# Performance work log

Measured on AMD Instinct MI355X. Metric: run time of the kernel, lower is better.

The kernel has to match this reference:

```python
import itertools
import jax, jax.numpy as jnp
import numpy as np

H, W, DIM, NH, WS = 64, 64, 384, 12, 7
HD = DIM // NH            # head dim = key_dim (attn_ratio=1)
N = WS * WS               # tokens per window
SCALE = HD ** -0.5
EPS = 1e-5
BATCH = 4
HID = int(DIM * 4.0)


def _bias_idxs():
    points = list(itertools.product(range(WS), range(WS)))
    offsets, idxs = {}, []
    for p1 in points:
        for p2 in points:
            off = (abs(p1[0] - p2[0]), abs(p1[1] - p2[1]))
            if off not in offsets:
                offsets[off] = len(offsets)
            idxs.append(offsets[off])
    return np.asarray(idxs, dtype=np.int32).reshape(N, N)

BIAS_IDXS = _bias_idxs()              # [N, N] static
NUM_OFFSETS = int(BIAS_IDXS.max()) + 1  # 49 for a 7x7 window


def setup_inputs() -> dict:
    key = jax.random.key(0)
    ks = jax.random.split(key, 10)
    rn = lambda k, shp, s=0.02: jax.random.normal(k, shp, jnp.float32) * s
    return {
        "x": jax.random.normal(ks[0], (BATCH, H * W, DIM), jnp.float32),
        "ln1_g": jnp.ones((DIM,), jnp.float32),
        "ln1_b": jnp.zeros((DIM,), jnp.float32),
        "qkv_w": rn(ks[1], (DIM, 3 * DIM)),
        "qkv_b": jnp.zeros((3 * DIM,), jnp.float32),
        "proj_w": rn(ks[2], (DIM, DIM)),
        "proj_b": jnp.zeros((DIM,), jnp.float32),
        "attn_bias": rn(ks[3], (NH, NUM_OFFSETS), 0.1),
        "conv_w": rn(ks[4], (DIM, 1, 3, 3), 0.1),  # depthwise OIHW
        "bn_g": jnp.ones((DIM,), jnp.float32),
        "bn_b": jnp.zeros((DIM,), jnp.float32),
        "bn_mean": rn(ks[5], (DIM,), 0.05),
        "bn_var": jax.random.uniform(ks[6], (DIM,), jnp.float32, 0.5, 1.5),
        "ln2_g": jnp.ones((DIM,), jnp.float32),
        "ln2_b": jnp.zeros((DIM,), jnp.float32),
        "fc1_w": rn(ks[7], (DIM, HID)),
        "fc1_b": jnp.zeros((HID,), jnp.float32),
        "fc2_w": rn(ks[8], (HID, DIM)),
        "fc2_b": jnp.zeros((DIM,), jnp.float32),
    }


def _ln(x, g, b):
    m = x.mean(-1, keepdims=True)
    v = jnp.var(x, axis=-1, keepdims=True)
    return (x - m) * jax.lax.rsqrt(v + EPS) * g + b


def reference(x, ln1_g, ln1_b, qkv_w, qkv_b, proj_w, proj_b, attn_bias,
              conv_w, bn_g, bn_b, bn_mean, bn_var, ln2_g, ln2_b,
              fc1_w, fc1_b, fc2_w, fc2_b):
    b, hw, c = x.shape
    res = x
    # --- window partition with padding ---
    pad_b = (-H) % WS
    pad_r = (-W) % WS
    pH, pW = H + pad_b, W + pad_r
    nH, nW = pH // WS, pW // WS
    xw = x.reshape(b, H, W, c)
    xw = jnp.pad(xw, ((0, 0), (0, pad_b), (0, pad_r), (0, 0)))
    xw = xw.reshape(b, nH, WS, nW, WS, c).transpose(0, 1, 3, 2, 4, 5)
    xw = xw.reshape(b * nH * nW, N, c)  # [Bw, N, C]
    # --- attention (pre-LN, relative position bias) ---
    xn = _ln(xw, ln1_g, ln1_b)
    qkv = (xn @ qkv_w + qkv_b).reshape(-1, N, NH, 3 * HD)
    q, k, v = jnp.split(qkv, [HD, 2 * HD], axis=-1)  # each [Bw, N, NH, HD]
    bias = attn_bias[:, BIAS_IDXS]                    # [NH, N, N]
    scores = jnp.einsum('bnhd,bmhd->bhnm', q, k) * SCALE + bias
    a = jax.nn.softmax(scores, axis=-1)
    o = jnp.einsum('bhnm,bmhd->bnhd', a, v).reshape(-1, N, NH * HD)
    xw = o @ proj_w + proj_b
    # --- window reverse + unpad ---
    xw = xw.reshape(b, nH, nW, WS, WS, c).transpose(0, 1, 3, 2, 4, 5)
    xw = xw.reshape(b, pH, pW, c)[:, :H, :W].reshape(b, hw, c)
    x = res + xw
    # --- depthwise 3x3 conv + BatchNorm (eval) ---
    xc = x.transpose(0, 2, 1).reshape(b, c, H, W)
    xc = jax.lax.conv_general_dilated(
        xc, conv_w, (1, 1), ((1, 1), (1, 1)),
        feature_group_count=c,
        dimension_numbers=('NCHW', 'OIHW', 'NCHW'))
    xc = (xc - bn_mean[:, None, None]) * jax.lax.rsqrt(bn_var[:, None, None] + EPS) \
         * bn_g[:, None, None] + bn_b[:, None, None]
    x = xc.reshape(b, c, hw).transpose(0, 2, 1)
    # --- MLP (pre-LN, GELU) with residual ---
    h1 = jax.nn.gelu(_ln(x, ln2_g, ln2_b) @ fc1_w + fc1_b, approximate=False)
    return x + (h1 @ fc2_w + fc2_b)
```

## Files before the change

kernel.cpp:

```cpp
#include <hip/hip_runtime.h>
#include <cstdint>


typedef __bf16 bf16x8 __attribute__((ext_vector_type(8)));
typedef __bf16 bf16x4 __attribute__((ext_vector_type(4)));
typedef float  f32x4  __attribute__((ext_vector_type(4)));

#define DIM_    384
#define QKVD    1152
#define HIDD    1536
#define NTOK    49
#define NWIN    400
#define MPAD    19712
#define MREAL   19600
#define TOKENS  16384
#define SCALE_  0.17677669529663689f
#define EPS_    1e-5f

#define B_LN1   9856
#define B_QKV   1728
#define B_PROJ  576
#define B_FC1   2304
#define B_FC2   2304
#define B_CONV  14
#define B_BIAS  192
#define B_TOTAL (B_LN1 + B_QKV + B_PROJ + B_FC1 + B_FC2 + B_CONV + B_BIAS)

__device__ __forceinline__ void gload_lds16(const void* g, void* l) {
  __builtin_amdgcn_global_load_lds(
      (__attribute__((address_space(1))) void*)g,
      (__attribute__((address_space(3))) void*)l, 16, 0, 0);
}

__device__ __forceinline__ float gelu_fast(float v) {
  float t2 = v * (1.5957691216057308f + 0.07135481627f * v * v);
  return v * __builtin_amdgcn_rcpf(1.f + __expf(-t2));
}

__global__ __launch_bounds__(256) void prep_all(
    const float* __restrict__ x, const float* __restrict__ ln1_g,
    const float* __restrict__ ln1_b, __bf16* __restrict__ xn,
    const float* __restrict__ qkv_w,  __bf16* __restrict__ wqkv,
    const float* __restrict__ proj_w, __bf16* __restrict__ wproj,
    const float* __restrict__ fc1_w,  __bf16* __restrict__ wfc1,
    const float* __restrict__ fc2_w,  __bf16* __restrict__ wfc2,
    const float* __restrict__ conv_w, float* __restrict__ wconv,
    const float* __restrict__ attn_b, float* __restrict__ bm) {
  int b = blockIdx.x;
  int tid = threadIdx.x;

  if (b < B_LN1) {
    int sub = tid >> 7, tl = tid & 127;
    int t = b * 2 + sub;
    __bf16* orow = xn + (long)t * DIM_;
    int kind;
    int bb = 0, r = 0, c = 0;
    if (t >= MREAL) kind = 2;
    else {
      int win = t / NTOK, tt = t % NTOK;
      bb = win / 100;
      int rem = win % 100;
      r = (rem / 10) * 7 + tt / 7;
      c = (rem % 10) * 7 + tt % 7;
      kind = (r >= 64 || c >= 64) ? 1 : 0;
    }
    float v0 = 0.f, v1 = 0.f, v2 = 0.f;
    if (kind == 0) {
      const float* xr = x + ((long)bb * 4096 + r * 64 + c) * DIM_;
      v0 = xr[tl]; v1 = xr[tl + 128]; v2 = xr[tl + 256];
    }
    float s = v0 + v1 + v2, s2 = v0 * v0 + v1 * v1 + v2 * v2;
    for (int off = 32; off; off >>= 1) { s += __shfl_down(s, off); s2 += __shfl_down(s2, off); }
    __shared__ float red[2][4];
    if ((tl & 63) == 0) { red[sub][tl >> 6] = s; red[sub][2 + (tl >> 6)] = s2; }
    __syncthreads();
    float S = red[sub][0] + red[sub][1], S2 = red[sub][2] + red[sub][3];
    float m  = S * (1.f / DIM_);
    float rs = rsqrtf(S2 * (1.f / DIM_) - m * m + EPS_);
    if (kind == 0) {
      orow[tl]       = (__bf16)((v0 - m) * rs * ln1_g[tl]       + ln1_b[tl]);
      orow[tl + 128] = (__bf16)((v1 - m) * rs * ln1_g[tl + 128] + ln1_b[tl + 128]);
      orow[tl + 256] = (__bf16)((v2 - m) * rs * ln1_g[tl + 256] + ln1_b[tl + 256]);
    } else if (kind == 1) {
      orow[tl]       = (__bf16)ln1_b[tl];
      orow[tl + 128] = (__bf16)ln1_b[tl + 128];
      orow[tl + 256] = (__bf16)ln1_b[tl + 256];
    } else {
      orow[tl] = (__bf16)0.f; orow[tl + 128] = (__bf16)0.f; orow[tl + 256] = (__bf16)0.f;
    }
    return;
  }
  b -= B_LN1;
  if (b < B_QKV) {
    int id = b * 256 + tid;
    int k = id % DIM_; int n = id / DIM_;
    wqkv[id] = (__bf16)qkv_w[(long)k * QKVD + n];
    return;
  }
  b -= B_QKV;
  if (b < B_PROJ) {
    int id = b * 256 + tid;
    int k = id % DIM_; int n = id / DIM_;
    wproj[id] = (__bf16)proj_w[(long)k * DIM_ + n];
    return;
  }
  b -= B_PROJ;
  if (b < B_FC1) {
    int id = b * 256 + tid;
    int k = id % DIM_; int n = id / DIM_;
    wfc1[id] = (__bf16)fc1_w[(long)k * HIDD + n];
    return;
  }
  b -= B_FC1;
  if (b < B_FC2) {
    int id = b * 256 + tid;
    int k = id % HIDD; int n = id / HIDD;
    wfc2[id] = (__bf16)fc2_w[(long)k * DIM_ + n];
    return;
  }
  b -= B_FC2;
  if (b < B_CONV) {
    int id = b * 256 + tid;
    if (id < 3456) {
      int ch = id / 9, k = id % 9;
      wconv[k * DIM_ + ch] = conv_w[id];
    }
    return;
  }
  b -= B_CONV;
  {
    int id = b * 256 + tid;
    int h = id >> 12, q = (id >> 6) & 63, kk = id & 63;
    float v;
    if (kk >= NTOK)      v = -1e30f;
    else if (q >= NTOK)  v = 0.f;
    else {
      int idx = abs(q / 7 - kk / 7) * 7 + abs(q % 7 - kk % 7);
      v = attn_b[h * NTOK + idx];
    }
    bm[id] = v;
  }
}

__global__ __launch_bounds__(384) void conv_bn_ln2(
    const float* __restrict__ x1, const float* __restrict__ wT,
    const float* __restrict__ bng, const float* __restrict__ bnb,
    const float* __restrict__ mean, const float* __restrict__ var,
    const float* __restrict__ g2, const float* __restrict__ b2,
    float* __restrict__ x2, __bf16* __restrict__ xln2) {
  int tid = threadIdx.x;
  int p = tid / 96, g = tid % 96;
  int pix = blockIdx.x * 4 + p;
  int bb = pix >> 12, rc = pix & 4095;
  int r = rc >> 6, c = rc & 63;
  int ch = g << 2;

  f32x4 acc = (f32x4){0.f, 0.f, 0.f, 0.f};
  #pragma unroll
  for (int dr = -1; dr <= 1; dr++) {
    int rr = r + dr;
    if (rr < 0 || rr >= 64) continue;
    #pragma unroll
    for (int dc = -1; dc <= 1; dc++) {
      int cc = c + dc;
      if (cc < 0 || cc >= 64) continue;
      f32x4 xv = *(const f32x4*)(x1 + ((long)bb * 4096 + rr * 64 + cc) * DIM_ + ch);
      f32x4 wv = *(const f32x4*)(wT + ((dr + 1) * 3 + (dc + 1)) * DIM_ + ch);
      acc += xv * wv;
    }
  }

  f32x4 gv = *(const f32x4*)(bng + ch);
  f32x4 vv = *(const f32x4*)(var + ch);
  f32x4 mv = *(const f32x4*)(mean + ch);
  f32x4 bv = *(const f32x4*)(bnb + ch);
  f32x4 y;
  #pragma unroll
  for (int j = 0; j < 4; j++) {
    float sc = gv[j] * rsqrtf(vv[j] + EPS_);
    y[j] = acc[j] * sc + (bv[j] - mv[j] * sc);
  }
  *(f32x4*)(x2 + (long)pix * DIM_ + ch) = y;

  __shared__ float pS[4][96], pS2[4][96], mS[4], rS[4];
  pS[p][g]  = y[0] + y[1] + y[2] + y[3];
  pS2[p][g] = y[0] * y[0] + y[1] * y[1] + y[2] * y[2] + y[3] * y[3];
  __syncthreads();
  if (g < 32) {
    float a  = pS[p][g]  + pS[p][g + 32]  + pS[p][g + 64];
    float a2 = pS2[p][g] + pS2[p][g + 32] + pS2[p][g + 64];
    #pragma unroll
    for (int off = 1; off < 32; off <<= 1) {
      a  += __shfl_xor(a, off);
      a2 += __shfl_xor(a2, off);
    }
    if (g == 0) {
      float m = a * (1.f / DIM_);
      mS[p] = m;
      rS[p] = rsqrtf(a2 * (1.f / DIM_) - m * m + EPS_);
    }
  }
  __syncthreads();
  float m = mS[p], rs = rS[p];
  f32x4 gg = *(const f32x4*)(g2 + ch);
  f32x4 b2v = *(const f32x4*)(b2 + ch);
  bf16x4 ov;
  #pragma unroll
  for (int j = 0; j < 4; j++) ov[j] = (__bf16)((y[j] - m) * rs * gg[j] + b2v[j]);
  *(bf16x4*)(xln2 + (long)pix * DIM_ + ch) = ov;
}

__global__ __launch_bounds__(64) void attn_mfma(const __bf16* __restrict__ qkv,
                                                const float* __restrict__ bm,
                                                __bf16* __restrict__ o) {
  int blk = blockIdx.x;
  int win = blk / 12, h = blk % 12;
  int lane = threadIdx.x;
  int quad = lane >> 4, l16 = lane & 15;

  __shared__ __align__(16) __bf16 Vt[32][72];
  __shared__ __align__(16) __bf16 P[64][72];

  const __bf16* base = qkv + (long)win * NTOK * QKVD + h * 96;

  bf16x8 qf[4], kf[4];
  #pragma unroll
  for (int t = 0; t < 4; t++) {
    const __bf16* rp = base + (long)(t * 16 + l16) * QKVD + quad * 8;
    qf[t] = *(const bf16x8*)(rp);
    kf[t] = *(const bf16x8*)(rp + 32);
  }
  {
    const __bf16* vp = base + (long)lane * QKVD + 64;
    bf16x8 vv[4];
    #pragma unroll
    for (int i = 0; i < 4; i++) vv[i] = *(const bf16x8*)(vp + i * 8);
    #pragma unroll
    for (int i = 0; i < 4; i++)
      #pragma unroll
      for (int j = 0; j < 8; j++) Vt[i * 8 + j][lane] = vv[i][j];
  }

  f32x4 S[4][4];
  #pragma unroll
  for (int i = 0; i < 4; i++)
    #pragma unroll
    for (int j = 0; j < 4; j++) S[i][j] = (f32x4){0.f, 0.f, 0.f, 0.f};
  #pragma unroll
  for (int mt = 0; mt < 4; mt++)
    #pragma unroll
    for (int nt = 0; nt < 4; nt++)
      S[mt][nt] = __builtin_amdgcn_mfma_f32_16x16x32_bf16(qf[mt], kf[nt], S[mt][nt], 0, 0, 0);

  const float* bmh = bm + h * 4096;
  #pragma unroll
  for (int mt = 0; mt < 4; mt++)
    #pragma unroll
    for (int r = 0; r < 4; r++) {
      int q = mt * 16 + quad * 4 + r;
      #pragma unroll
      for (int nt = 0; nt < 4; nt++)
        S[mt][nt][r] = S[mt][nt][r] * SCALE_ + bmh[q * 64 + nt * 16 + l16];
    }

  #pragma unroll
  for (int mt = 0; mt < 4; mt++)
    #pragma unroll
    for (int r = 0; r < 4; r++) {
      float mx = fmaxf(fmaxf(S[mt][0][r], S[mt][1][r]), fmaxf(S[mt][2][r], S[mt][3][r]));
      #pragma unroll
      for (int off = 1; off < 16; off <<= 1) mx = fmaxf(mx, __shfl_xor(mx, off));
      float sum = 0.f;
      #pragma unroll
      for (int nt = 0; nt < 4; nt++) {
        float e = __expf(S[mt][nt][r] - mx);
        S[mt][nt][r] = e;
        sum += e;
      }
      #pragma unroll
      for (int off = 1; off < 16; off <<= 1) sum += __shfl_xor(sum, off);
      float inv = 1.f / sum;
      #pragma unroll
      for (int nt = 0; nt < 4; nt++) S[mt][nt][r] *= inv;
    }

  #pragma unroll
  for (int mt = 0; mt < 4; mt++)
    #pragma unroll
    for (int r = 0; r < 4; r++) {
      int q = mt * 16 + quad * 4 + r;
      #pragma unroll
      for (int nt = 0; nt < 4; nt++)
        P[q][nt * 16 + l16] = (__bf16)S[mt][nt][r];
    }
  __syncthreads();

  f32x4 O[4][2];
  #pragma unroll
  for (int i = 0; i < 4; i++)
    #pragma unroll
    for (int j = 0; j < 2; j++) O[i][j] = (f32x4){0.f, 0.f, 0.f, 0.f};
  #pragma unroll
  for (int kt = 0; kt < 2; kt++) {
    bf16x8 pf[4], vf[2];
    #pragma unroll
    for (int mt = 0; mt < 4; mt++)
      pf[mt] = *(const bf16x8*)(&P[mt * 16 + l16][kt * 32 + quad * 8]);
    #pragma unroll
    for (int nt = 0; nt < 2; nt++)
      vf[nt] = *(const bf16x8*)(&Vt[nt * 16 + l16][kt * 32 + quad * 8]);
    #pragma unroll
    for (int mt = 0; mt < 4; mt++)
      #pragma unroll
      for (int nt = 0; nt < 2; nt++)
        O[mt][nt] = __builtin_amdgcn_mfma_f32_16x16x32_bf16(pf[mt], vf[nt], O[mt][nt], 0, 0, 0);
  }

  __bf16* ob = o + (long)win * NTOK * DIM_ + h * 32;
  #pragma unroll
  for (int mt = 0; mt < 4; mt++)
    #pragma unroll
    for (int r = 0; r < 4; r++) {
      int q = mt * 16 + quad * 4 + r;
      if (q < NTOK) {
        #pragma unroll
        for (int nt = 0; nt < 2; nt++)
          ob[(long)q * DIM_ + nt * 16 + l16] = (__bf16)O[mt][nt][r];
      }
    }
}

template <int MODE, int TN>
__global__ void __launch_bounds__(256)
gemm_bf16(const __bf16* __restrict__ A, const __bf16* __restrict__ Bt,
          const float* __restrict__ bias, int K, int N,
          float* __restrict__ outf, __bf16* __restrict__ outb,
          const float* __restrict__ res) {
  constexpr int NT = TN / 32;
  __shared__ __align__(16) __bf16 sA[2][128 * 32];
  __shared__ __align__(16) __bf16 sB[2][TN * 32];
  int tid = threadIdx.x, lane = tid & 63, wid = tid >> 6;
  int wm = wid >> 1, wn = wid & 1;
  int quad = lane >> 4, l16 = lane & 15;
  long tileM = (long)blockIdx.x * 128;
  long tileN = (long)blockIdx.y * TN;

  f32x4 acc[4][NT];
  #pragma unroll
  for (int i = 0; i < 4; i++)
    #pragma unroll
    for (int j = 0; j < NT; j++) acc[i][j] = (f32x4){0.f, 0.f, 0.f, 0.f};

  int rr = wid * 16 + (lane >> 2);
  const __bf16* gA = A  + (tileM + rr) * (long)K + ((lane & 3) << 3);
  const __bf16* gB = Bt + (tileN + rr) * (long)K + ((lane & 3) << 3);
  const long rowskip = 64 * (long)K;

  for (int k0 = 0; k0 < K; k0 += 64) {
    #pragma unroll
    for (int h = 0; h < 2; h++) {
      const int ko = k0 + h * 32;
      gload_lds16(gA + ko,           &sA[h][wid << 9]);
      gload_lds16(gA + ko + rowskip, &sA[h][(wid + 4) << 9]);
      gload_lds16(gB + ko,           &sB[h][wid << 9]);
      if (TN == 128)
        gload_lds16(gB + ko + rowskip, &sB[h][(wid + 4) << 9]);
    }
    __syncthreads();
    #pragma unroll
    for (int h = 0; h < 2; h++) {
      bf16x8 af[4], bfr[NT];
      #pragma unroll
      for (int mt = 0; mt < 4; mt++)
        af[mt] = *(const bf16x8*)(&sA[h][((wm * 64 + mt * 16 + l16) << 5) + (quad << 3)]);
      #pragma unroll
      for (int nt = 0; nt < NT; nt++)
        bfr[nt] = *(const bf16x8*)(&sB[h][((wn * (TN / 2) + nt * 16 + l16) << 5) + (quad << 3)]);
      #pragma unroll
      for (int mt = 0; mt < 4; mt++)
        #pragma unroll
        for (int nt = 0; nt < NT; nt++)
          acc[mt][nt] = __builtin_amdgcn_mfma_f32_16x16x32_bf16(af[mt], bfr[nt], acc[mt][nt], 0, 0, 0);
    }
    __syncthreads();
  }

  float bcol[NT];
  #pragma unroll
  for (int nt = 0; nt < NT; nt++) bcol[nt] = bias[tileN + wn * (TN / 2) + nt * 16 + l16];

  #pragma unroll
  for (int mt = 0; mt < 4; mt++) {
    #pragma unroll
    for (int r = 0; r < 4; r++) {
      long row = tileM + wm * 64 + mt * 16 + quad * 4 + r;
      if (MODE == 0) {
        __bf16* orow = outb + row * (long)N;
        #pragma unroll
        for (int nt = 0; nt < NT; nt++)
          orow[tileN + wn * (TN / 2) + nt * 16 + l16] = (__bf16)(acc[mt][nt][r] + bcol[nt]);
      } else if (MODE == 1) {
        if (row < MREAL) {
          int r32 = (int)row;
          int win = r32 / NTOK, t = r32 % NTOK;
          int rem = win % 100;
          int pr = (rem / 10) * 7 + t / 7;
          int pc = (rem % 10) * 7 + t % 7;
          if (pr < 64 && pc < 64) {
            long po = ((long)(win / 100) * 4096 + pr * 64 + pc) * DIM_;
            #pragma unroll
            for (int nt = 0; nt < NT; nt++) {
              long col = tileN + wn * (TN / 2) + nt * 16 + l16;
              outf[po + col] = res[po + col] + acc[mt][nt][r] + bcol[nt];
            }
          }
        }
      } else if (MODE == 2) {
        __bf16* orow = outb + row * (long)N;
        #pragma unroll
        for (int nt = 0; nt < NT; nt++) {
          float v = acc[mt][nt][r] + bcol[nt];
          orow[tileN + wn * (TN / 2) + nt * 16 + l16] = (__bf16)gelu_fast(v);
        }
      } else {
        float* orow = outf + row * (long)N;
        const float* rrow = res + row * (long)N;
        #pragma unroll
        for (int nt = 0; nt < NT; nt++) {
          long col = tileN + wn * (TN / 2) + nt * 16 + l16;
          orow[col] = acc[mt][nt][r] + bcol[nt] + rrow[col];
        }
      }
    }
  }
}

extern "C" void kernel_launch(void* const* d_in, const int* in_sizes, int n_in,
                              void* d_out, int out_size, void* d_ws, size_t ws_size,
                              hipStream_t stream) {
  const float* x       = (const float*)d_in[0];
  const float* ln1_g   = (const float*)d_in[1];
  const float* ln1_b   = (const float*)d_in[2];
  const float* qkv_w   = (const float*)d_in[3];
  const float* qkv_b   = (const float*)d_in[4];
  const float* proj_w  = (const float*)d_in[5];
  const float* proj_b  = (const float*)d_in[6];
  const float* attn_b  = (const float*)d_in[7];
  const float* conv_w  = (const float*)d_in[8];
  const float* bn_g    = (const float*)d_in[9];
  const float* bn_b    = (const float*)d_in[10];
  const float* bn_mean = (const float*)d_in[11];
  const float* bn_var  = (const float*)d_in[12];
  const float* ln2_g   = (const float*)d_in[13];
  const float* ln2_b   = (const float*)d_in[14];
  const float* fc1_w   = (const float*)d_in[15];
  const float* fc1_b   = (const float*)d_in[16];
  const float* fc2_w   = (const float*)d_in[17];
  const float* fc2_b   = (const float*)d_in[18];

  char* p = (char*)d_ws;
  __bf16* WQKV = (__bf16*)p;  p += 884736;
  __bf16* WPROJ = (__bf16*)p; p += 294912;
  __bf16* WFC1 = (__bf16*)p;  p += 1179648;
  __bf16* WFC2 = (__bf16*)p;  p += 1179648;
  float*  WCONV = (float*)p;  p += 13824;
  char* region = p;           p += 75694080;
  float* X1 = (float*)p;      p += 25165824;
  float* X2 = (float*)p;      p += 25165824;
  __bf16* XN   = (__bf16*)region;
  __bf16* QKVB = (__bf16*)(region + 15138816);
  __bf16* OBUF = (__bf16*)(region + 60555264);
  __bf16* XLN2 = (__bf16*)region;
  __bf16* H1   = (__bf16*)(region + 15138816);
  float*  BM   = X1;
  float* OUT = (float*)d_out;

  prep_all<<<B_TOTAL, 256, 0, stream>>>(x, ln1_g, ln1_b, XN,
                                        qkv_w, WQKV, proj_w, WPROJ,
                                        fc1_w, WFC1, fc2_w, WFC2,
                                        conv_w, WCONV, attn_b, BM);

  gemm_bf16<0, 128><<<dim3(MPAD / 128, QKVD / 128), 256, 0, stream>>>(
      XN, WQKV, qkv_b, DIM_, QKVD, nullptr, QKVB, nullptr);

  attn_mfma<<<NWIN * 12, 64, 0, stream>>>(QKVB, BM, OBUF);

  gemm_bf16<1, 64><<<dim3(MPAD / 128, DIM_ / 64), 256, 0, stream>>>(
      OBUF, WPROJ, proj_b, DIM_, DIM_, X1, nullptr, x);

  conv_bn_ln2<<<TOKENS / 4, 384, 0, stream>>>(X1, WCONV, bn_g, bn_b, bn_mean, bn_var,
                                              ln2_g, ln2_b, X2, XLN2);

  gemm_bf16<2, 128><<<dim3(TOKENS / 128, HIDD / 128), 256, 0, stream>>>(
      XLN2, WFC1, fc1_b, DIM_, HIDD, nullptr, H1, nullptr);

  gemm_bf16<3, 64><<<dim3(TOKENS / 128, DIM_ / 64), 256, 0, stream>>>(
      H1, WFC2, fc2_b, HIDD, DIM_, OUT, nullptr, X2);
}
```

Before: 296.7 us.

## Replace LDS-staged GEMM with direct global-to-register MFMA fragment loads

Drops the shared-memory staging (global_load_lds plus two barriers per K step) from all four GEMMs. Each wave now loads its MFMA A and B fragments straight from global memory into registers, and K becomes a template constant so the loop can be unrolled. This removes LDS traffic and synchronisation, but tiles are no longer shared across waves, so each wave re-reads data that other waves also fetch and relies on L1/L2 hits. The per-lane 16-byte loads are also strided by a full row, which gives poorer coalescing than the old staged loads.

```diff
diff --git a/kernel.cpp b/kernel.cpp
--- a/kernel.cpp
+++ b/kernel.cpp
@@ -25,12 +25,6 @@
 #define B_CONV  14
 #define B_BIAS  192
 #define B_TOTAL (B_LN1 + B_QKV + B_PROJ + B_FC1 + B_FC2 + B_CONV + B_BIAS)
-
-__device__ __forceinline__ void gload_lds16(const void* g, void* l) {
-  __builtin_amdgcn_global_load_lds(
-      (__attribute__((address_space(1))) void*)g,
-      (__attribute__((address_space(3))) void*)l, 16, 0, 0);
-}
 
 __device__ __forceinline__ float gelu_fast(float v) {
   float t2 = v * (1.5957691216057308f + 0.07135481627f * v * v);
@@ -330,15 +324,13 @@
     }
 }
 
-template <int MODE, int TN>
+template <int MODE, int TN, int KK>
 __global__ void __launch_bounds__(256)
-gemm_bf16(const __bf16* __restrict__ A, const __bf16* __restrict__ Bt,
-          const float* __restrict__ bias, int K, int N,
-          float* __restrict__ outf, __bf16* __restrict__ outb,
-          const float* __restrict__ res) {
+gemm_direct(const __bf16* __restrict__ A, const __bf16* __restrict__ Bt,
+            const float* __restrict__ bias, int N,
+            float* __restrict__ outf, __bf16* __restrict__ outb,
+            const float* __restrict__ res) {
   constexpr int NT = TN / 32;
-  __shared__ __align__(16) __bf16 sA[2][128 * 32];
-  __shared__ __align__(16) __bf16 sB[2][TN * 32];
   int tid = threadIdx.x, lane = tid & 63, wid = tid >> 6;
   int wm = wid >> 1, wn = wid & 1;
   int quad = lane >> 4, l16 = lane & 15;
@@ -351,38 +343,23 @@
     #pragma unroll
     for (int j = 0; j < NT; j++) acc[i][j] = (f32x4){0.f, 0.f, 0.f, 0.f};
 
-  int rr = wid * 16 + (lane >> 2);
-  const __bf16* gA = A  + (tileM + rr) * (long)K + ((lane & 3) << 3);
-  const __bf16* gB = Bt + (tileN + rr) * (long)K + ((lane & 3) << 3);
-  const long rowskip = 64 * (long)K;
-
-  for (int k0 = 0; k0 < K; k0 += 64) {
-    #pragma unroll
-    for (int h = 0; h < 2; h++) {
-      const int ko = k0 + h * 32;
-      gload_lds16(gA + ko,           &sA[h][wid << 9]);
-      gload_lds16(gA + ko + rowskip, &sA[h][(wid + 4) << 9]);
-      gload_lds16(gB + ko,           &sB[h][wid << 9]);
-      if (TN == 128)
-        gload_lds16(gB + ko + rowskip, &sB[h][(wid + 4) << 9]);
-    }
-    __syncthreads();
-    #pragma unroll
-    for (int h = 0; h < 2; h++) {
-      bf16x8 af[4], bfr[NT];
-      #pragma unroll
-      for (int mt = 0; mt < 4; mt++)
-        af[mt] = *(const bf16x8*)(&sA[h][((wm * 64 + mt * 16 + l16) << 5) + (quad << 3)]);
+  const __bf16* aBase = A  + (tileM + wm * 64 + l16) * (long)KK + quad * 8;
+  const __bf16* bBase = Bt + (tileN + wn * (TN / 2) + l16) * (long)KK + quad * 8;
+
+  #pragma unroll 2
+  for (int k0 = 0; k0 < KK; k0 += 32) {
+    bf16x8 af[4], bfr[NT];
+    #pragma unroll
+    for (int mt = 0; mt < 4; mt++)
+      af[mt] = *(const bf16x8*)(aBase + (long)mt * 16 * KK + k0);
+    #pragma unroll
+    for (int nt = 0; nt < NT; nt++)
+      bfr[nt] = *(const bf16x8*)(bBase + (long)nt * 16 * KK + k0);
+    #pragma unroll
+    for (int mt = 0; mt < 4; mt++)
       #pragma unroll
       for (int nt = 0; nt < NT; nt++)
-        bfr[nt] = *(const bf16x8*)(&sB[h][((wn * (TN / 2) + nt * 16 + l16) << 5) + (quad << 3)]);
-      #pragma unroll
-      for (int mt = 0; mt < 4; mt++)
-        #pragma unroll
-        for (int nt = 0; nt < NT; nt++)
-          acc[mt][nt] = __builtin_amdgcn_mfma_f32_16x16x32_bf16(af[mt], bfr[nt], acc[mt][nt], 0, 0, 0);
-    }
-    __syncthreads();
+        acc[mt][nt] = __builtin_amdgcn_mfma_f32_16x16x32_bf16(af[mt], bfr[nt], acc[mt][nt], 0, 0, 0);
   }
 
   float bcol[NT];
@@ -480,20 +457,20 @@
                                         fc1_w, WFC1, fc2_w, WFC2,
                                         conv_w, WCONV, attn_b, BM);
 
-  gemm_bf16<0, 128><<<dim3(MPAD / 128, QKVD / 128), 256, 0, stream>>>(
-      XN, WQKV, qkv_b, DIM_, QKVD, nullptr, QKVB, nullptr);
+  gemm_direct<0, 128, DIM_><<<dim3(MPAD / 128, QKVD / 128), 256, 0, stream>>>(
+      XN, WQKV, qkv_b, QKVD, nullptr, QKVB, nullptr);
 
   attn_mfma<<<NWIN * 12, 64, 0, stream>>>(QKVB, BM, OBUF);
 
-  gemm_bf16<1, 64><<<dim3(MPAD / 128, DIM_ / 64), 256, 0, stream>>>(
-      OBUF, WPROJ, proj_b, DIM_, DIM_, X1, nullptr, x);
+  gemm_direct<1, 64, DIM_><<<dim3(MPAD / 128, DIM_ / 64), 256, 0, stream>>>(
+      OBUF, WPROJ, proj_b, DIM_, X1, nullptr, x);
 
   conv_bn_ln2<<<TOKENS / 4, 384, 0, stream>>>(X1, WCONV, bn_g, bn_b, bn_mean, bn_var,
                                               ln2_g, ln2_b, X2, XLN2);
 
-  gemm_bf16<2, 128><<<dim3(TOKENS / 128, HIDD / 128), 256, 0, stream>>>(
-      XLN2, WFC1, fc1_b, DIM_, HIDD, nullptr, H1, nullptr);
-
-  gemm_bf16<3, 64><<<dim3(TOKENS / 128, DIM_ / 64), 256, 0, stream>>>(
-      H1, WFC2, fc2_b, HIDD, DIM_, OUT, nullptr, X2);
-}
+  gemm_direct<2, 128, DIM_><<<dim3(TOKENS / 128, HIDD / 128), 256, 0, stream>>>(
+      XLN2, WFC1, fc1_b, HIDD, nullptr, H1, nullptr);
+
+  gemm_direct<3, 64, HIDD><<<dim3(TOKENS / 128, DIM_ / 64), 256, 0, stream>>>(
+      H1, WFC2, fc2_b, DIM_, OUT, nullptr, X2);
+}
```

Measured after the change: 457.1 us. 54.1% more time.

## Compute QKV and proj GEMMs on unpadded tokens, gather windows inside attention

Applied to the files above, without the earlier changes.

QKV and projection GEMMs now run over the 16384 real tokens in image order plus one shared pad row holding the LN1 bias, instead of the 19712-row padded window layout. The attention kernel maps each window token to its image row (or the pad row) when loading Q/K/V and scatters its output straight to image order, so the proj GEMM can use the plain residual epilogue. This removes the padded-row GEMM work and the LN1 permutation. Separately, the GEMM K-loop drops from 64 per iteration with two LDS stages to a single 32-wide stage, which means more barriers per K step.

```diff
diff --git a/kernel.cpp b/kernel.cpp
--- a/kernel.cpp
+++ b/kernel.cpp
@@ -11,20 +11,21 @@
 #define HIDD    1536
 #define NTOK    49
 #define NWIN    400
-#define MPAD    19712
-#define MREAL   19600
 #define TOKENS  16384
+#define PADROW  16384
+#define MQKV    16512
 #define SCALE_  0.17677669529663689f
 #define EPS_    1e-5f
 
-#define B_LN1   9856
+#define B_LN1   8192
+#define B_PADR  1
 #define B_QKV   1728
 #define B_PROJ  576
 #define B_FC1   2304
 #define B_FC2   2304
 #define B_CONV  14
 #define B_BIAS  192
-#define B_TOTAL (B_LN1 + B_QKV + B_PROJ + B_FC1 + B_FC2 + B_CONV + B_BIAS)
+#define B_TOTAL (B_LN1 + B_PADR + B_QKV + B_PROJ + B_FC1 + B_FC2 + B_CONV + B_BIAS)
 
 __device__ __forceinline__ void gload_lds16(const void* g, void* l) {
   __builtin_amdgcn_global_load_lds(
@@ -51,24 +52,9 @@
 
   if (b < B_LN1) {
     int sub = tid >> 7, tl = tid & 127;
-    int t = b * 2 + sub;
-    __bf16* orow = xn + (long)t * DIM_;
-    int kind;
-    int bb = 0, r = 0, c = 0;
-    if (t >= MREAL) kind = 2;
-    else {
-      int win = t / NTOK, tt = t % NTOK;
-      bb = win / 100;
-      int rem = win % 100;
-      r = (rem / 10) * 7 + tt / 7;
-      c = (rem % 10) * 7 + tt % 7;
-      kind = (r >= 64 || c >= 64) ? 1 : 0;
-    }
-    float v0 = 0.f, v1 = 0.f, v2 = 0.f;
-    if (kind == 0) {
-      const float* xr = x + ((long)bb * 4096 + r * 64 + c) * DIM_;
-      v0 = xr[tl]; v1 = xr[tl + 128]; v2 = xr[tl + 256];
-    }
+    long t = (long)b * 2 + sub;
+    const float* xr = x + t * DIM_;
+    float v0 = xr[tl], v1 = xr[tl + 128], v2 = xr[tl + 256];
     float s = v0 + v1 + v2, s2 = v0 * v0 + v1 * v1 + v2 * v2;
     for (int off = 32; off; off >>= 1) { s += __shfl_down(s, off); s2 += __shfl_down(s2, off); }
     __shared__ float red[2][4];
@@ -77,20 +63,19 @@
     float S = red[sub][0] + red[sub][1], S2 = red[sub][2] + red[sub][3];
     float m  = S * (1.f / DIM_);
     float rs = rsqrtf(S2 * (1.f / DIM_) - m * m + EPS_);
-    if (kind == 0) {
-      orow[tl]       = (__bf16)((v0 - m) * rs * ln1_g[tl]       + ln1_b[tl]);
-      orow[tl + 128] = (__bf16)((v1 - m) * rs * ln1_g[tl + 128] + ln1_b[tl + 128]);
-      orow[tl + 256] = (__bf16)((v2 - m) * rs * ln1_g[tl + 256] + ln1_b[tl + 256]);
-    } else if (kind == 1) {
-      orow[tl]       = (__bf16)ln1_b[tl];
-      orow[tl + 128] = (__bf16)ln1_b[tl + 128];
-      orow[tl + 256] = (__bf16)ln1_b[tl + 256];
-    } else {
-      orow[tl] = (__bf16)0.f; orow[tl + 128] = (__bf16)0.f; orow[tl + 256] = (__bf16)0.f;
-    }
+    __bf16* orow = xn + t * DIM_;
+    orow[tl]       = (__bf16)((v0 - m) * rs * ln1_g[tl]       + ln1_b[tl]);
+    orow[tl + 128] = (__bf16)((v1 - m) * rs * ln1_g[tl + 128] + ln1_b[tl + 128]);
+    orow[tl + 256] = (__bf16)((v2 - m) * rs * ln1_g[tl + 256] + ln1_b[tl + 256]);
     return;
   }
   b -= B_LN1;
+  if (b < B_PADR) {
+    for (int i = tid; i < DIM_; i += 256)
+      xn[(long)PADROW * DIM_ + i] = (__bf16)ln1_b[i];
+    return;
+  }
+  b -= B_PADR;
   if (b < B_QKV) {
     int id = b * 256 + tid;
     int k = id % DIM_; int n = id / DIM_;
@@ -215,23 +200,33 @@
                                                 __bf16* __restrict__ o) {
   int blk = blockIdx.x;
   int win = blk / 12, h = blk % 12;
+  int bb = win / 100, rem = win % 100;
+  int wy = rem / 10, wx = rem % 10;
   int lane = threadIdx.x;
   int quad = lane >> 4, l16 = lane & 15;
 
   __shared__ __align__(16) __bf16 Vt[32][72];
   __shared__ __align__(16) __bf16 P[64][72];
 
-  const __bf16* base = qkv + (long)win * NTOK * QKVD + h * 96;
+  const __bf16* base = qkv + h * 96;
 
   bf16x8 qf[4], kf[4];
   #pragma unroll
-  for (int t = 0; t < 4; t++) {
-    const __bf16* rp = base + (long)(t * 16 + l16) * QKVD + quad * 8;
-    qf[t] = *(const bf16x8*)(rp);
-    kf[t] = *(const bf16x8*)(rp + 32);
+  for (int mt = 0; mt < 4; mt++) {
+    int t = mt * 16 + l16;
+    int ty = t / 7, tx = t % 7;
+    int r = wy * 7 + ty, c = wx * 7 + tx;
+    int row = (t < NTOK && r < 64 && c < 64) ? (bb * 4096 + r * 64 + c) : PADROW;
+    const __bf16* rp = base + (long)row * QKVD + quad * 8;
+    qf[mt] = *(const bf16x8*)(rp);
+    kf[mt] = *(const bf16x8*)(rp + 32);
   }
   {
-    const __bf16* vp = base + (long)lane * QKVD + 64;
+    int t = lane;
+    int ty = t / 7, tx = t % 7;
+    int r = wy * 7 + ty, c = wx * 7 + tx;
+    int row = (t < NTOK && r < 64 && c < 64) ? (bb * 4096 + r * 64 + c) : PADROW;
+    const __bf16* vp = base + (long)row * QKVD + 64;
     bf16x8 vv[4];
     #pragma unroll
     for (int i = 0; i < 4; i++) vv[i] = *(const bf16x8*)(vp + i * 8);
@@ -316,16 +311,20 @@
         O[mt][nt] = __builtin_amdgcn_mfma_f32_16x16x32_bf16(pf[mt], vf[nt], O[mt][nt], 0, 0, 0);
   }
 
-  __bf16* ob = o + (long)win * NTOK * DIM_ + h * 32;
   #pragma unroll
   for (int mt = 0; mt < 4; mt++)
     #pragma unroll
     for (int r = 0; r < 4; r++) {
       int q = mt * 16 + quad * 4 + r;
       if (q < NTOK) {
-        #pragma unroll
-        for (int nt = 0; nt < 2; nt++)
-          ob[(long)q * DIM_ + nt * 16 + l16] = (__bf16)O[mt][nt][r];
+        int ty = q / 7, tx = q % 7;
+        int rr = wy * 7 + ty, cc = wx * 7 + tx;
+        if (rr < 64 && cc < 64) {
+          __bf16* ob = o + ((long)bb * 4096 + rr * 64 + cc) * DIM_ + h * 32;
+          #pragma unroll
+          for (int nt = 0; nt < 2; nt++)
+            ob[nt * 16 + l16] = (__bf16)O[mt][nt][r];
+        }
       }
     }
 }
@@ -337,8 +336,8 @@
           float* __restrict__ outf, __bf16* __restrict__ outb,
           const float* __restrict__ res) {
   constexpr int NT = TN / 32;
-  __shared__ __align__(16) __bf16 sA[2][128 * 32];
-  __shared__ __align__(16) __bf16 sB[2][TN * 32];
+  __shared__ __align__(16) __bf16 sA[128 * 32];
+  __shared__ __align__(16) __bf16 sB[TN * 32];
   int tid = threadIdx.x, lane = tid & 63, wid = tid >> 6;
   int wm = wid >> 1, wn = wid & 1;
   int quad = lane >> 4, l16 = lane & 15;
@@ -356,32 +355,25 @@
   const __bf16* gB = Bt + (tileN + rr) * (long)K + ((lane & 3) << 3);
   const long rowskip = 64 * (long)K;
 
-  for (int k0 = 0; k0 < K; k0 += 64) {
-    #pragma unroll
-    for (int h = 0; h < 2; h++) {
-      const int ko = k0 + h * 32;
-      gload_lds16(gA + ko,           &sA[h][wid << 9]);
-      gload_lds16(gA + ko + rowskip, &sA[h][(wid + 4) << 9]);
-      gload_lds16(gB + ko,           &sB[h][wid << 9]);
-      if (TN == 128)
-        gload_lds16(gB + ko + rowskip, &sB[h][(wid + 4) << 9]);
-    }
+  for (int k0 = 0; k0 < K; k0 += 32) {
+    gload_lds16(gA + k0,           sA + (wid << 9));
+    gload_lds16(gA + k0 + rowskip, sA + ((wid + 4) << 9));
+    gload_lds16(gB + k0,           sB + (wid << 9));
+    if (TN == 128)
+      gload_lds16(gB + k0 + rowskip, sB + ((wid + 4) << 9));
     __syncthreads();
-    #pragma unroll
-    for (int h = 0; h < 2; h++) {
-      bf16x8 af[4], bfr[NT];
-      #pragma unroll
-      for (int mt = 0; mt < 4; mt++)
-        af[mt] = *(const bf16x8*)(&sA[h][((wm * 64 + mt * 16 + l16) << 5) + (quad << 3)]);
+    bf16x8 af[4], bfr[NT];
+    #pragma unroll
+    for (int mt = 0; mt < 4; mt++)
+      af[mt] = *(const bf16x8*)(sA + ((wm * 64 + mt * 16 + l16) << 5) + (quad << 3));
+    #pragma unroll
+    for (int nt = 0; nt < NT; nt++)
+      bfr[nt] = *(const bf16x8*)(sB + ((wn * (TN / 2) + nt * 16 + l16) << 5) + (quad << 3));
+    #pragma unroll
+    for (int mt = 0; mt < 4; mt++)
       #pragma unroll
       for (int nt = 0; nt < NT; nt++)
-        bfr[nt] = *(const bf16x8*)(&sB[h][((wn * (TN / 2) + nt * 16 + l16) << 5) + (quad << 3)]);
-      #pragma unroll
-      for (int mt = 0; mt < 4; mt++)
-        #pragma unroll
-        for (int nt = 0; nt < NT; nt++)
-          acc[mt][nt] = __builtin_amdgcn_mfma_f32_16x16x32_bf16(af[mt], bfr[nt], acc[mt][nt], 0, 0, 0);
-    }
+        acc[mt][nt] = __builtin_amdgcn_mfma_f32_16x16x32_bf16(af[mt], bfr[nt], acc[mt][nt], 0, 0, 0);
     __syncthreads();
   }
 
@@ -399,22 +391,6 @@
         #pragma unroll
         for (int nt = 0; nt < NT; nt++)
           orow[tileN + wn * (TN / 2) + nt * 16 + l16] = (__bf16)(acc[mt][nt][r] + bcol[nt]);
-      } else if (MODE == 1) {
-        if (row < MREAL) {
-          int r32 = (int)row;
-          int win = r32 / NTOK, t = r32 % NTOK;
-          int rem = win % 100;
-          int pr = (rem / 10) * 7 + t / 7;
-          int pc = (rem % 10) * 7 + t % 7;
-          if (pr < 64 && pc < 64) {
-            long po = ((long)(win / 100) * 4096 + pr * 64 + pc) * DIM_;
-            #pragma unroll
-            for (int nt = 0; nt < NT; nt++) {
-              long col = tileN + wn * (TN / 2) + nt * 16 + l16;
-              outf[po + col] = res[po + col] + acc[mt][nt][r] + bcol[nt];
-            }
-          }
-        }
       } else if (MODE == 2) {
         __bf16* orow = outb + row * (long)N;
         #pragma unroll
@@ -464,14 +440,14 @@
   __bf16* WFC1 = (__bf16*)p;  p += 1179648;
   __bf16* WFC2 = (__bf16*)p;  p += 1179648;
   float*  WCONV = (float*)p;  p += 13824;
-  char* region = p;           p += 75694080;
+  char* region = p;           p += 63307776;
   float* X1 = (float*)p;      p += 25165824;
   float* X2 = (float*)p;      p += 25165824;
   __bf16* XN   = (__bf16*)region;
-  __bf16* QKVB = (__bf16*)(region + 15138816);
-  __bf16* OBUF = (__bf16*)(region + 60555264);
+  __bf16* QKVB = (__bf16*)(region + 12681216);
+  __bf16* OBUF = (__bf16*)(region + 50724864);
   __bf16* XLN2 = (__bf16*)region;
-  __bf16* H1   = (__bf16*)(region + 15138816);
+  __bf16* H1   = (__bf16*)(region + 12681216);
   float*  BM   = X1;
   float* OUT = (float*)d_out;
 
@@ -480,12 +456,12 @@
                                         fc1_w, WFC1, fc2_w, WFC2,
                                         conv_w, WCONV, attn_b, BM);
 
-  gemm_bf16<0, 128><<<dim3(MPAD / 128, QKVD / 128), 256, 0, stream>>>(
+  gemm_bf16<0, 128><<<dim3(MQKV / 128, QKVD / 128), 256, 0, stream>>>(
       XN, WQKV, qkv_b, DIM_, QKVD, nullptr, QKVB, nullptr);
 
   attn_mfma<<<NWIN * 12, 64, 0, stream>>>(QKVB, BM, OBUF);
 
-  gemm_bf16<1, 64><<<dim3(MPAD / 128, DIM_ / 64), 256, 0, stream>>>(
+  gemm_bf16<3, 64><<<dim3(TOKENS / 128, DIM_ / 64), 256, 0, stream>>>(
       OBUF, WPROJ, proj_b, DIM_, DIM_, X1, nullptr, x);
 
   conv_bn_ln2<<<TOKENS / 4, 384, 0, stream>>>(X1, WCONV, bn_g, bn_b, bn_mean, bn_var,
```

Measured after the change: 287.2 us. 3.2% less time.
